# Performance work log

Measured on AMD Instinct MI355X. Metric: run time of the kernel, lower is better.

Reference implementation:

```python
import jax, jax.numpy as jnp
import numpy as np

EPS = 1e-9  # avoids nan gradient of sqrt at r=0 (self-pairs)


def setup_inputs() -> dict:
    key = jax.random.key(0)
    k1, k2, k3 = jax.random.split(key, 3)
    B, N, C_IN, C_OUT, R = 1, 768, 16, 16, 8
    features = jax.random.normal(k1, (B, N, C_IN), dtype=jnp.float32)
    geometry = jax.random.normal(k2, (B, N, 3), dtype=jnp.float32)
    # learned radial-kernel weights: [basis, c_out, c_in]
    W = jax.random.normal(k3, (R, C_OUT, C_IN), dtype=jnp.float32) / np.sqrt(R * C_IN)
    mu = jnp.linspace(0.0, 3.0, R).astype(jnp.float32)       # RBF centers
    gamma = jnp.full((R,), 2.0, dtype=jnp.float32)            # RBF inverse widths
    return {"features": features, "geometry": geometry, "W": W,
            "mu": mu, "gamma": gamma, "n_norm": N}


def reference(features, geometry, W, mu, gamma, n_norm):
    # rel[z,a,b,:] = geometry[z,b] - geometry[z,a]   (rb - ra, as in the torch code)
    rel = geometry[:, None, :, :] - geometry[:, :, None, :]          # [B,a,b,3]
    d = jnp.sqrt(jnp.sum(rel * rel, axis=-1) + EPS)                  # [B,a,b]
    # radial basis expansion of pairwise distance: [B,a,b,R]
    rbf = jnp.exp(-gamma * (d[..., None] - mu) ** 2)
    # k[z,a,b,i,j] = sum_r rbf[z,a,b,r] * W[r,i,j];  k /= sqrt(n_norm)
    rbf = rbf / jnp.sqrt(jnp.asarray(n_norm, dtype=features.dtype))
    # fused kernel-build + contraction (avoids materializing [B,a,b,i,j])
    out = jnp.einsum('zabr,rij,zbj->zai', rbf, W, features)          # [B,a,c_out]
    return out
```

## Files before the change

kernel.cpp:

```cpp
#include <hip/hip_runtime.h>

#define NPTS 768
#define TPB  256

__global__ __launch_bounds__(TPB) void rbf_conv_kernel(
        const float* __restrict__ feat,
        const float* __restrict__ geom,
        const float* __restrict__ Wp,
        const float* __restrict__ mup,
        const float* __restrict__ gmp,
        const int*   __restrict__ nn,
        float* __restrict__ outp)
{
    __shared__ __align__(16) float zone[NPTS * 12];
    __shared__ float gx[NPTS], gy[NPTS], gz[NPTS];
    __shared__ float Tred[128];
    __shared__ float Pp[64];

    const int t = threadIdx.x;
    const int a = blockIdx.x;

    for (int b = t; b < NPTS; b += TPB) {
        gx[b] = geom[b * 3 + 0];
        gy[b] = geom[b * 3 + 1];
        gz[b] = geom[b * 3 + 2];
    }
    const float ax = geom[a * 3 + 0];
    const float ay = geom[a * 3 + 1];
    const float az = geom[a * 3 + 2];
    float muv[8], ngv[8];
#pragma unroll
    for (int r = 0; r < 8; ++r) { muv[r] = mup[r]; ngv[r] = -gmp[r]; }
    const float rn = rsqrtf((float)nn[0]);

    __syncthreads();

    for (int b = t; b < NPTS; b += TPB) {
        float dx = gx[b] - ax, dy = gy[b] - ay, dz = gz[b] - az;
        float d = sqrtf(fmaf(dx, dx, fmaf(dy, dy, fmaf(dz, dz, 1e-9f))));
        float e[8];
#pragma unroll
        for (int r = 0; r < 8; ++r) {
            float t0 = d - muv[r];
            e[r] = __expf(ngv[r] * t0 * t0) * rn;
        }
        *(float4*)(zone + b * 12 + 0) = make_float4(e[0], e[1], e[2], e[3]);
        *(float4*)(zone + b * 12 + 4) = make_float4(e[4], e[5], e[6], e[7]);
    }
    __syncthreads();

    const int jq = t & 3;
    const int g  = t >> 2;
    float acc[8][4];
#pragma unroll
    for (int r = 0; r < 8; ++r)
#pragma unroll
        for (int jj = 0; jj < 4; ++jj) acc[r][jj] = 0.f;

    const float4* feat4 = (const float4*)feat;
#pragma unroll
    for (int k = 0; k < 12; ++k) {
        const int b = g + (k << 6);
        const float4 ra = *(const float4*)(zone + b * 12 + 0);
        const float4 rb = *(const float4*)(zone + b * 12 + 4);
        const float4 fv = feat4[b * 4 + jq];
        float rr[8] = { ra.x, ra.y, ra.z, ra.w, rb.x, rb.y, rb.z, rb.w };
        float fj[4] = { fv.x, fv.y, fv.z, fv.w };
#pragma unroll
        for (int r = 0; r < 8; ++r)
#pragma unroll
            for (int jj = 0; jj < 4; ++jj)
                acc[r][jj] = fmaf(rr[r], fj[jj], acc[r][jj]);
    }
    __syncthreads();

    float* Tp = zone;
#pragma unroll
    for (int r = 0; r < 8; ++r) {
        *(float4*)(Tp + g * 132 + r * 16 + jq * 4) =
            make_float4(acc[r][0], acc[r][1], acc[r][2], acc[r][3]);
    }
    __syncthreads();

    if (t < 128) {
        const int r = t >> 4, j = t & 15;
        float s = 0.f;
        const float* base = Tp + r * 16 + j;
        for (int gg = 0; gg < 64; ++gg) s += base[gg * 132];
        Tred[t] = s;
    }
    __syncthreads();

    if (t < 64) {
        const int i = t & 15, q = t >> 4;
        float s = 0.f;
#pragma unroll
        for (int m = 0; m < 32; ++m) {
            const int rj = q * 32 + m;
            const int r = rj >> 4, j = rj & 15;
            s = fmaf(Wp[r * 256 + i * 16 + j], Tred[rj], s);
        }
        Pp[t] = s;
    }
    __syncthreads();

    if (t < 16) {
        const float s = Pp[t] + Pp[t + 16] + Pp[t + 32] + Pp[t + 48];
        outp[a * 16 + t] = s;
    }
}

extern "C" void kernel_launch(void* const* d_in, const int* in_sizes, int n_in,
                              void* d_out, int out_size, void* d_ws, size_t ws_size,
                              hipStream_t stream) {
    const float* feat = (const float*)d_in[0];
    const float* geom = (const float*)d_in[1];
    const float* Wp   = (const float*)d_in[2];
    const float* mup  = (const float*)d_in[3];
    const float* gmp  = (const float*)d_in[4];
    const int*   nn   = (const int*)d_in[5];
    float* outp = (float*)d_out;
    rbf_conv_kernel<<<dim3(NPTS), dim3(TPB), 0, stream>>>(feat, geom, Wp, mup, gmp, nn, outp);
}
```

Baseline: 68.53 us.

## Precontract W with features per b and split b-range across blocks

Reorders the contraction so each block first computes G[b,r,i] = sum_j W[r,i,j]*f[b,j] for a 12-point chunk of b. Each thread then handles one target point a and accumulates rbf times G directly into 16 outputs. Work is split into 64 b-chunks by 12 a-groups, with partial sums written to workspace and summed by a second reduce kernel. This removes the heavy per-a shared-memory reduction and the serial W contraction tail. In exchange it costs a second launch and about 3 MB of partial-sum traffic through global memory.

```diff
diff --git a/kernel.cpp b/kernel.cpp
--- a/kernel.cpp
+++ b/kernel.cpp
@@ -1,30 +1,38 @@
 #include <hip/hip_runtime.h>
 
-#define NPTS 768
-#define TPB  256
+#define NPTS   768
+#define TPB    256
+#define CHUNKS 64
+#define BPB    12
+#define BPW    3
+#define OUTSZ  (NPTS * 16)
+#define RSTR   20
 
-__global__ __launch_bounds__(TPB) void rbf_conv_kernel(
+__global__ __launch_bounds__(TPB) void rbf_main(
         const float* __restrict__ feat,
         const float* __restrict__ geom,
         const float* __restrict__ Wp,
         const float* __restrict__ mup,
         const float* __restrict__ gmp,
         const int*   __restrict__ nn,
-        float* __restrict__ outp)
+        float* __restrict__ partial)
 {
-    __shared__ __align__(16) float zone[NPTS * 12];
-    __shared__ float gx[NPTS], gy[NPTS], gz[NPTS];
-    __shared__ float Tred[128];
-    __shared__ float Pp[64];
+    __shared__ __align__(16) float Gs[BPB * 128];
+    __shared__ __align__(16) float red[4 * 64 * RSTR];
+    __shared__ __align__(16) float fS[BPB * 16];
+    __shared__ float gB[BPB * 3];
 
-    const int t = threadIdx.x;
-    const int a = blockIdx.x;
+    const int t    = threadIdx.x;
+    const int cid  = blockIdx.x % CHUNKS;
+    const int ag   = blockIdx.x / CHUNKS;
+    const int b0   = cid * BPB;
+    const int lane = t & 63;
+    const int w    = t >> 6;
+    const int a    = ag * 64 + lane;
 
-    for (int b = t; b < NPTS; b += TPB) {
-        gx[b] = geom[b * 3 + 0];
-        gy[b] = geom[b * 3 + 1];
-        gz[b] = geom[b * 3 + 2];
-    }
+    if (t < BPB * 16) fS[t] = feat[b0 * 16 + t];
+    if (t < BPB * 3)  gB[t] = geom[b0 * 3 + t];
+
     const float ax = geom[a * 3 + 0];
     const float ay = geom[a * 3 + 1];
     const float az = geom[a * 3 + 2];
@@ -35,79 +43,98 @@
 
     __syncthreads();
 
-    for (int b = t; b < NPTS; b += TPB) {
-        float dx = gx[b] - ax, dy = gy[b] - ay, dz = gz[b] - az;
-        float d = sqrtf(fmaf(dx, dx, fmaf(dy, dy, fmaf(dz, dz, 1e-9f))));
-        float e[8];
 #pragma unroll
-        for (int r = 0; r < 8; ++r) {
-            float t0 = d - muv[r];
-            e[r] = __expf(ngv[r] * t0 * t0) * rn;
-        }
-        *(float4*)(zone + b * 12 + 0) = make_float4(e[0], e[1], e[2], e[3]);
-        *(float4*)(zone + b * 12 + 4) = make_float4(e[4], e[5], e[6], e[7]);
+    for (int m = 0; m < 6; ++m) {
+        const int idx = t + m * TPB;
+        const int bb  = idx >> 7;
+        const int k   = idx & 127;
+        const float4 f0 = *(const float4*)(fS + bb * 16 + 0);
+        const float4 f1 = *(const float4*)(fS + bb * 16 + 4);
+        const float4 f2 = *(const float4*)(fS + bb * 16 + 8);
+        const float4 f3 = *(const float4*)(fS + bb * 16 + 12);
+        const float4 w0 = *(const float4*)(Wp + k * 16 + 0);
+        const float4 w1 = *(const float4*)(Wp + k * 16 + 4);
+        const float4 w2 = *(const float4*)(Wp + k * 16 + 8);
+        const float4 w3 = *(const float4*)(Wp + k * 16 + 12);
+        float s = 0.f;
+        s = fmaf(f0.x, w0.x, s); s = fmaf(f0.y, w0.y, s);
+        s = fmaf(f0.z, w0.z, s); s = fmaf(f0.w, w0.w, s);
+        s = fmaf(f1.x, w1.x, s); s = fmaf(f1.y, w1.y, s);
+        s = fmaf(f1.z, w1.z, s); s = fmaf(f1.w, w1.w, s);
+        s = fmaf(f2.x, w2.x, s); s = fmaf(f2.y, w2.y, s);
+        s = fmaf(f2.z, w2.z, s); s = fmaf(f2.w, w2.w, s);
+        s = fmaf(f3.x, w3.x, s); s = fmaf(f3.y, w3.y, s);
+        s = fmaf(f3.z, w3.z, s); s = fmaf(f3.w, w3.w, s);
+        Gs[idx] = s * rn;
     }
     __syncthreads();
 
-    const int jq = t & 3;
-    const int g  = t >> 2;
-    float acc[8][4];
+    float acc[16];
 #pragma unroll
-    for (int r = 0; r < 8; ++r)
+    for (int i = 0; i < 16; ++i) acc[i] = 0.f;
+
 #pragma unroll
-        for (int jj = 0; jj < 4; ++jj) acc[r][jj] = 0.f;
+    for (int q = 0; q < BPW; ++q) {
+        const int bb = w * BPW + q;
+        const float dx = gB[bb * 3 + 0] - ax;
+        const float dy = gB[bb * 3 + 1] - ay;
+        const float dz = gB[bb * 3 + 2] - az;
+        const float d  = sqrtf(fmaf(dx, dx, fmaf(dy, dy, fmaf(dz, dz, 1e-9f))));
+        float rbf[8];
+#pragma unroll
+        for (int r = 0; r < 8; ++r) {
+            const float t0 = d - muv[r];
+            rbf[r] = __expf(ngv[r] * t0 * t0);
+        }
+#pragma unroll
+        for (int r = 0; r < 8; ++r) {
+            const float4 g0 = *(const float4*)(Gs + bb * 128 + r * 16 + 0);
+            const float4 g1 = *(const float4*)(Gs + bb * 128 + r * 16 + 4);
+            const float4 g2 = *(const float4*)(Gs + bb * 128 + r * 16 + 8);
+            const float4 g3 = *(const float4*)(Gs + bb * 128 + r * 16 + 12);
+            acc[0]  = fmaf(rbf[r], g0.x, acc[0]);  acc[1]  = fmaf(rbf[r], g0.y, acc[1]);
+            acc[2]  = fmaf(rbf[r], g0.z, acc[2]);  acc[3]  = fmaf(rbf[r], g0.w, acc[3]);
+            acc[4]  = fmaf(rbf[r], g1.x, acc[4]);  acc[5]  = fmaf(rbf[r], g1.y, acc[5]);
+            acc[6]  = fmaf(rbf[r], g1.z, acc[6]);  acc[7]  = fmaf(rbf[r], g1.w, acc[7]);
+            acc[8]  = fmaf(rbf[r], g2.x, acc[8]);  acc[9]  = fmaf(rbf[r], g2.y, acc[9]);
+            acc[10] = fmaf(rbf[r], g2.z, acc[10]); acc[11] = fmaf(rbf[r], g2.w, acc[11]);
+            acc[12] = fmaf(rbf[r], g3.x, acc[12]); acc[13] = fmaf(rbf[r], g3.y, acc[13]);
+            acc[14] = fmaf(rbf[r], g3.z, acc[14]); acc[15] = fmaf(rbf[r], g3.w, acc[15]);
+        }
+    }
 
-    const float4* feat4 = (const float4*)feat;
+    float* rrow = red + (w * 64 + lane) * RSTR;
 #pragma unroll
-    for (int k = 0; k < 12; ++k) {
-        const int b = g + (k << 6);
-        const float4 ra = *(const float4*)(zone + b * 12 + 0);
-        const float4 rb = *(const float4*)(zone + b * 12 + 4);
-        const float4 fv = feat4[b * 4 + jq];
-        float rr[8] = { ra.x, ra.y, ra.z, ra.w, rb.x, rb.y, rb.z, rb.w };
-        float fj[4] = { fv.x, fv.y, fv.z, fv.w };
-#pragma unroll
-        for (int r = 0; r < 8; ++r)
-#pragma unroll
-            for (int jj = 0; jj < 4; ++jj)
-                acc[r][jj] = fmaf(rr[r], fj[jj], acc[r][jj]);
-    }
+    for (int i = 0; i < 16; i += 4)
+        *(float4*)(rrow + i) = make_float4(acc[i], acc[i + 1], acc[i + 2], acc[i + 3]);
     __syncthreads();
 
-    float* Tp = zone;
 #pragma unroll
-    for (int r = 0; r < 8; ++r) {
-        *(float4*)(Tp + g * 132 + r * 16 + jq * 4) =
-            make_float4(acc[r][0], acc[r][1], acc[r][2], acc[r][3]);
+    for (int m = 0; m < 4; ++m) {
+        const int idx = t + m * TPB;
+        const int al  = idx >> 4;
+        const int i   = idx & 15;
+        const float s = red[(0 * 64 + al) * RSTR + i]
+                      + red[(1 * 64 + al) * RSTR + i]
+                      + red[(2 * 64 + al) * RSTR + i]
+                      + red[(3 * 64 + al) * RSTR + i];
+        partial[cid * OUTSZ + ag * 1024 + idx] = s;
     }
-    __syncthreads();
+}
 
-    if (t < 128) {
-        const int r = t >> 4, j = t & 15;
-        float s = 0.f;
-        const float* base = Tp + r * 16 + j;
-        for (int gg = 0; gg < 64; ++gg) s += base[gg * 132];
-        Tred[t] = s;
+__global__ __launch_bounds__(256) void rbf_reduce(
+        const float* __restrict__ partial, float* __restrict__ outp)
+{
+    const int o = blockIdx.x * 256 + threadIdx.x;
+    float s0 = 0.f, s1 = 0.f, s2 = 0.f, s3 = 0.f;
+#pragma unroll
+    for (int c = 0; c < CHUNKS; c += 4) {
+        s0 += partial[(c + 0) * OUTSZ + o];
+        s1 += partial[(c + 1) * OUTSZ + o];
+        s2 += partial[(c + 2) * OUTSZ + o];
+        s3 += partial[(c + 3) * OUTSZ + o];
     }
-    __syncthreads();
-
-    if (t < 64) {
-        const int i = t & 15, q = t >> 4;
-        float s = 0.f;
-#pragma unroll
-        for (int m = 0; m < 32; ++m) {
-            const int rj = q * 32 + m;
-            const int r = rj >> 4, j = rj & 15;
-            s = fmaf(Wp[r * 256 + i * 16 + j], Tred[rj], s);
-        }
-        Pp[t] = s;
-    }
-    __syncthreads();
-
-    if (t < 16) {
-        const float s = Pp[t] + Pp[t + 16] + Pp[t + 32] + Pp[t + 48];
-        outp[a * 16 + t] = s;
-    }
+    outp[o] = (s0 + s1) + (s2 + s3);
 }
 
 extern "C" void kernel_launch(void* const* d_in, const int* in_sizes, int n_in,
@@ -119,6 +146,9 @@
     const float* mup  = (const float*)d_in[3];
     const float* gmp  = (const float*)d_in[4];
     const int*   nn   = (const int*)d_in[5];
-    float* outp = (float*)d_out;
-    rbf_conv_kernel<<<dim3(NPTS), dim3(TPB), 0, stream>>>(feat, geom, Wp, mup, gmp, nn, outp);
+    float* outp    = (float*)d_out;
+    float* partial = (float*)d_ws;
+
+    rbf_main<<<dim3(NPTS), dim3(TPB), 0, stream>>>(feat, geom, Wp, mup, gmp, nn, partial);
+    rbf_reduce<<<dim3(OUTSZ / 256), dim3(256), 0, stream>>>(partial, outp);
 }
```

New measurement: 71.70 us. 1.05x slower.

## Replace shared-memory reduction with wave shuffles and drop geometry staging

Applied to the files above, without the earlier changes.

Partial sums over the 64 point-groups are now reduced inside each wavefront with xor shuffles, and only four lanes per wave write to a small per-wave buffer. This replaces the large shared-memory transpose and the serial 64-step reduction loop. Geometry is read straight from global memory instead of being staged in shared memory first, which removes two block barriers and some LDS use. The cost is 32 values times four shuffle steps per thread, plus uncoalesced strided global reads of geometry.

```diff
diff --git a/kernel.cpp b/kernel.cpp
--- a/kernel.cpp
+++ b/kernel.cpp
@@ -12,19 +12,15 @@
         const int*   __restrict__ nn,
         float* __restrict__ outp)
 {
-    __shared__ __align__(16) float zone[NPTS * 12];
-    __shared__ float gx[NPTS], gy[NPTS], gz[NPTS];
-    __shared__ float Tred[128];
+    __shared__ __align__(16) float rbfz[NPTS * 12];
+    __shared__ __align__(16) float Twave[4][128];
     __shared__ float Pp[64];
 
     const int t = threadIdx.x;
     const int a = blockIdx.x;
+    const int w = t >> 6;
+    const int l = t & 63;
 
-    for (int b = t; b < NPTS; b += TPB) {
-        gx[b] = geom[b * 3 + 0];
-        gy[b] = geom[b * 3 + 1];
-        gz[b] = geom[b * 3 + 2];
-    }
     const float ax = geom[a * 3 + 0];
     const float ay = geom[a * 3 + 1];
     const float az = geom[a * 3 + 2];
@@ -33,19 +29,19 @@
     for (int r = 0; r < 8; ++r) { muv[r] = mup[r]; ngv[r] = -gmp[r]; }
     const float rn = rsqrtf((float)nn[0]);
 
-    __syncthreads();
-
     for (int b = t; b < NPTS; b += TPB) {
-        float dx = gx[b] - ax, dy = gy[b] - ay, dz = gz[b] - az;
-        float d = sqrtf(fmaf(dx, dx, fmaf(dy, dy, fmaf(dz, dz, 1e-9f))));
+        const float dx = geom[b * 3 + 0] - ax;
+        const float dy = geom[b * 3 + 1] - ay;
+        const float dz = geom[b * 3 + 2] - az;
+        const float d  = sqrtf(fmaf(dx, dx, fmaf(dy, dy, fmaf(dz, dz, 1e-9f))));
         float e[8];
 #pragma unroll
         for (int r = 0; r < 8; ++r) {
-            float t0 = d - muv[r];
+            const float t0 = d - muv[r];
             e[r] = __expf(ngv[r] * t0 * t0) * rn;
         }
-        *(float4*)(zone + b * 12 + 0) = make_float4(e[0], e[1], e[2], e[3]);
-        *(float4*)(zone + b * 12 + 4) = make_float4(e[4], e[5], e[6], e[7]);
+        *(float4*)(rbfz + b * 12 + 0) = make_float4(e[0], e[1], e[2], e[3]);
+        *(float4*)(rbfz + b * 12 + 4) = make_float4(e[4], e[5], e[6], e[7]);
     }
     __syncthreads();
 
@@ -61,33 +57,35 @@
 #pragma unroll
     for (int k = 0; k < 12; ++k) {
         const int b = g + (k << 6);
-        const float4 ra = *(const float4*)(zone + b * 12 + 0);
-        const float4 rb = *(const float4*)(zone + b * 12 + 4);
+        const float4 ra = *(const float4*)(rbfz + b * 12 + 0);
+        const float4 rb = *(const float4*)(rbfz + b * 12 + 4);
         const float4 fv = feat4[b * 4 + jq];
-        float rr[8] = { ra.x, ra.y, ra.z, ra.w, rb.x, rb.y, rb.z, rb.w };
-        float fj[4] = { fv.x, fv.y, fv.z, fv.w };
+        const float rr[8] = { ra.x, ra.y, ra.z, ra.w, rb.x, rb.y, rb.z, rb.w };
+        const float fj[4] = { fv.x, fv.y, fv.z, fv.w };
 #pragma unroll
         for (int r = 0; r < 8; ++r)
 #pragma unroll
             for (int jj = 0; jj < 4; ++jj)
                 acc[r][jj] = fmaf(rr[r], fj[jj], acc[r][jj]);
     }
-    __syncthreads();
 
-    float* Tp = zone;
 #pragma unroll
-    for (int r = 0; r < 8; ++r) {
-        *(float4*)(Tp + g * 132 + r * 16 + jq * 4) =
-            make_float4(acc[r][0], acc[r][1], acc[r][2], acc[r][3]);
-    }
-    __syncthreads();
+    for (int r = 0; r < 8; ++r)
+#pragma unroll
+        for (int jj = 0; jj < 4; ++jj) {
+            float v = acc[r][jj];
+            v += __shfl_xor(v, 4);
+            v += __shfl_xor(v, 8);
+            v += __shfl_xor(v, 16);
+            v += __shfl_xor(v, 32);
+            acc[r][jj] = v;
+        }
 
-    if (t < 128) {
-        const int r = t >> 4, j = t & 15;
-        float s = 0.f;
-        const float* base = Tp + r * 16 + j;
-        for (int gg = 0; gg < 64; ++gg) s += base[gg * 132];
-        Tred[t] = s;
+    if (l < 4) {
+#pragma unroll
+        for (int r = 0; r < 8; ++r)
+            *(float4*)(&Twave[w][r * 16 + jq * 4]) =
+                make_float4(acc[r][0], acc[r][1], acc[r][2], acc[r][3]);
     }
     __syncthreads();
 
@@ -97,16 +95,16 @@
 #pragma unroll
         for (int m = 0; m < 32; ++m) {
             const int rj = q * 32 + m;
+            const float tv = Twave[0][rj] + Twave[1][rj] + Twave[2][rj] + Twave[3][rj];
             const int r = rj >> 4, j = rj & 15;
-            s = fmaf(Wp[r * 256 + i * 16 + j], Tred[rj], s);
+            s = fmaf(Wp[r * 256 + i * 16 + j], tv, s);
         }
         Pp[t] = s;
     }
     __syncthreads();
 
     if (t < 16) {
-        const float s = Pp[t] + Pp[t + 16] + Pp[t + 32] + Pp[t + 48];
-        outp[a * 16 + t] = s;
+        outp[a * 16 + t] = Pp[t] + Pp[t + 16] + Pp[t + 32] + Pp[t + 48];
     }
 }
 
```

Measured after the change: 71.25 us. 1.04x slower.
